# Kernel tuning notes

Hardware: AMD Instinct MI355X
Metric: run time of the kernel (lower is better)

The kernel has to match this reference:

```python
import jax, jax.numpy as jnp
import numpy as np

N_NODES = 100000
N_EDGES = 625000
EMB_DIM = 128
ALPHA = 0.8  # alpha in original; effective scale is alpha/2 = 0.4


def setup_inputs() -> dict:
    key = jax.random.key(0)
    k1, k2, k3, k4, k5 = jax.random.split(key, 5)
    x = jax.random.normal(k1, (N_NODES, EMB_DIM), dtype=jnp.float32)
    e = jax.random.normal(k2, (N_NODES, EMB_DIM), dtype=jnp.float32)
    hg_vals = jax.random.uniform(k3, (N_EDGES,), dtype=jnp.float32)
    hg_rows = jax.random.randint(k4, (N_EDGES,), 0, N_NODES, dtype=jnp.int32)
    hg_cols = jax.random.randint(k5, (N_EDGES,), 0, N_NODES, dtype=jnp.int32)
    t = jnp.zeros((), dtype=jnp.float32)
    return {"t": t, "x": x, "e": e, "hg_vals": hg_vals,
            "hg_rows": hg_rows, "hg_cols": hg_cols}


def reference(t, x, e, hg_vals, hg_rows, hg_cols):
    # f = spmm((alpha/2) * HG, x) - x + e, with alpha = 0.8 (constant per entry)
    n = x.shape[0]
    scale = ALPHA / 2.0
    # gather source node features per nonzero, scale by edge value
    msgs = (scale * hg_vals)[:, None] * x[hg_cols]          # [nnz, d]
    prop = jax.ops.segment_sum(msgs, hg_rows, num_segments=n)  # [N, d]
    return prop - x + e
```

## Files before the change

### kernel.cpp

```cpp
#include <hip/hip_runtime.h>
#include <hip/hip_fp16.h>


#define EMB_DIM 128
#define Q_SLOTS 32
#define CAP 16
#define OVF_MAX 8192
#define EPT 8

struct __align__(8) half4_t { __half2 a, b; };
typedef float f32x4 __attribute__((ext_vector_type(4)));
typedef unsigned long long u64;

__global__ void prep_kernel(const int* __restrict__ rows,
                            const int* __restrict__ cols,
                            const float* __restrict__ vals,
                            int* __restrict__ counts,
                            u64* __restrict__ slots,
                            int* __restrict__ ovf_cursor,
                            int4* __restrict__ ovf, int n_edges,
                            const f32x4* __restrict__ x4,
                            half4_t* __restrict__ xh4, int n_x4,
                            int bin_blocks)
{
    if ((int)blockIdx.x < bin_blocks) {
        const int T = bin_blocks * 256;
        const int t = blockIdx.x * 256 + threadIdx.x;
        for (int i0 = t; i0 < n_edges; i0 += T * EPT) {
            int   r[EPT], c[EPT];
            float v[EPT];
            bool  ok[EPT];
#pragma unroll
            for (int k = 0; k < EPT; ++k) {
                int i = i0 + k * T;
                ok[k] = (i < n_edges);
                if (ok[k]) { r[k] = rows[i]; c[k] = cols[i]; v[k] = vals[i]; }
            }
            int pos[EPT];
#pragma unroll
            for (int k = 0; k < EPT; ++k)
                if (ok[k]) pos[k] = atomicAdd(&counts[r[k]], 1);
#pragma unroll
            for (int k = 0; k < EPT; ++k) {
                if (!ok[k]) continue;
                u64 pv = (u64)(unsigned)c[k] |
                         ((u64)(unsigned)__float_as_int(0.4f * v[k]) << 32);
                if (pos[k] < CAP) {
                    slots[(size_t)r[k] * CAP + pos[k]] = pv;
                } else {
                    int o = atomicAdd(ovf_cursor, 1);
                    if (o < OVF_MAX)
                        ovf[o] = make_int4(r[k], c[k],
                                           __float_as_int(0.4f * v[k]), 0);
                }
            }
        }
    } else {
        long long j = ((long long)(blockIdx.x - bin_blocks) * 256 +
                       threadIdx.x) * 2;
        if (j < n_x4) {
            f32x4 f0 = x4[j];
            half4_t h0;
            h0.a = __floats2half2_rn(f0.x, f0.y);
            h0.b = __floats2half2_rn(f0.z, f0.w);
            xh4[j] = h0;
            if (j + 1 < n_x4) {
                f32x4 f1 = x4[j + 1];
                half4_t h1;
                h1.a = __floats2half2_rn(f1.x, f1.y);
                h1.b = __floats2half2_rn(f1.z, f1.w);
                xh4[j + 1] = h1;
            }
        }
    }
}

__global__ void gather_kernel(const half4_t* __restrict__ xh4,
                              const f32x4* __restrict__ e4,
                              const int* __restrict__ counts,
                              const u64* __restrict__ slots,
                              const int* __restrict__ ovf_cursor,
                              const int4* __restrict__ ovf,
                              f32x4* __restrict__ out4, int n_nodes)
{
    int tid = blockIdx.x * blockDim.x + threadIdx.x;
    int row = tid >> 5;
    int q   = tid & 31;
    if (row >= n_nodes) return;

    int cfull = counts[row];
    int n = (cfull < CAP) ? cfull : CAP;
    const u64* b = slots + (size_t)row * CAP;

    u64 pp = 0;
    if (q < n) pp = __builtin_nontemporal_load(b + q);
    int myc = (int)(pp & 0xffffffffULL);
    int myv = (int)(pp >> 32);

    float4 acc = make_float4(0.f, 0.f, 0.f, 0.f);
    int nm1 = n - 1;

    for (int base = 0; base < n; base += 8) {
        int   col[8];
        float v[8];
#pragma unroll
        for (int k = 0; k < 8; ++k) {
            int j  = base + k;
            int jc = (j < n) ? j : nm1;
            col[k] = __shfl(myc, jc, 32);
            int vi = __shfl(myv, jc, 32);
            v[k]   = (j < n) ? __int_as_float(vi) : 0.f;
        }
        half4_t hv[8];
#pragma unroll
        for (int k = 0; k < 8; ++k) {
            hv[k] = xh4[col[k] * Q_SLOTS + q];
        }
#pragma unroll
        for (int k = 0; k < 8; ++k) {
            float2 f0 = __half22float2(hv[k].a);
            float2 f1 = __half22float2(hv[k].b);
            acc.x = fmaf(v[k], f0.x, acc.x);
            acc.y = fmaf(v[k], f0.y, acc.y);
            acc.z = fmaf(v[k], f1.x, acc.z);
            acc.w = fmaf(v[k], f1.y, acc.w);
        }
    }

    if (cfull > CAP) {
        int cnt = *ovf_cursor;
        cnt = (cnt < OVF_MAX) ? cnt : OVF_MAX;
        for (int k = 0; k < cnt; ++k) {
            int4 en = ovf[k];
            if (en.x == row) {
                float vv = __int_as_float(en.z);
                half4_t hv = xh4[en.y * Q_SLOTS + q];
                float2 f0 = __half22float2(hv.a);
                float2 f1 = __half22float2(hv.b);
                acc.x = fmaf(vv, f0.x, acc.x);
                acc.y = fmaf(vv, f0.y, acc.y);
                acc.z = fmaf(vv, f1.x, acc.z);
                acc.w = fmaf(vv, f1.y, acc.w);
            }
        }
    }

    int idx = row * Q_SLOTS + q;
    half4_t hx = xh4[idx];
    float2 x0 = __half22float2(hx.a);
    float2 x1 = __half22float2(hx.b);
    f32x4 er = __builtin_nontemporal_load(e4 + idx);
    f32x4 o;
    o.x = acc.x + er.x - x0.x;
    o.y = acc.y + er.y - x0.y;
    o.z = acc.z + er.z - x1.x;
    o.w = acc.w + er.w - x1.y;
    __builtin_nontemporal_store(o, out4 + idx);
}

__global__ void build_chain_kernel(const int* __restrict__ rows,
                                   const int* __restrict__ cols,
                                   const float* __restrict__ vals,
                                   int* __restrict__ head,
                                   int4* __restrict__ nodes, int n_edges) {
    int i = blockIdx.x * blockDim.x + threadIdx.x;
    if (i >= n_edges) return;
    int r = rows[i];
    int prev = atomicExch(&head[r], i);
    nodes[i] = make_int4(cols[i], __float_as_int(0.4f * vals[i]), prev, 0);
}
__global__ void gather_chain_kernel(const float2* __restrict__ x2,
                                    const float2* __restrict__ e2,
                                    const int* __restrict__ head,
                                    const int4* __restrict__ nodes,
                                    float2* __restrict__ out2, int n_nodes) {
    int tid = blockIdx.x * blockDim.x + threadIdx.x;
    int row = tid >> 6, q = tid & 63;
    if (row >= n_nodes) return;
    float2 acc = make_float2(0.f, 0.f);
    int j = head[row];
    if (j >= 0) {
        int4 nd = nodes[j];
        for (;;) {
            int4 nd2;
            bool more = (nd.z >= 0);
            if (more) nd2 = nodes[nd.z];
            float v = __int_as_float(nd.y);
            float2 xv = x2[nd.x * 64 + q];
            acc.x = fmaf(v, xv.x, acc.x);
            acc.y = fmaf(v, xv.y, acc.y);
            if (!more) break;
            nd = nd2;
        }
    }
    int idx = row * 64 + q;
    float2 xr = x2[idx], er = e2[idx];
    out2[idx] = make_float2(acc.x + er.x - xr.x, acc.y + er.y - xr.y);
}

extern "C" void kernel_launch(void* const* d_in, const int* in_sizes, int n_in,
                              void* d_out, int out_size, void* d_ws, size_t ws_size,
                              hipStream_t stream) {
    const float* x    = (const float*)d_in[1];
    const float* e    = (const float*)d_in[2];
    const float* vals = (const float*)d_in[3];
    const int*   rows = (const int*)d_in[4];
    const int*   cols = (const int*)d_in[5];
    float* out = (float*)d_out;

    const int n_edges = in_sizes[3];
    const int n_nodes = in_sizes[1] / EMB_DIM;
    const int n_x4    = n_nodes * Q_SLOTS;

    size_t need_a = (size_t)OVF_MAX * sizeof(int4) +
                    (size_t)n_x4 * sizeof(half4_t) +
                    (size_t)n_nodes * CAP * sizeof(u64) +
                    (size_t)(n_nodes + 1) * sizeof(int);

    if (ws_size >= need_a) {
        int4*    ovf        = (int4*)d_ws;
        half4_t* xh4        = (half4_t*)(ovf + OVF_MAX);
        u64*     slots      = (u64*)(xh4 + (size_t)n_x4);
        int*     counts     = (int*)(slots + (size_t)n_nodes * CAP);
        int*     ovf_cursor = counts + n_nodes;

        hipMemsetAsync(counts, 0, (size_t)(n_nodes + 1) * sizeof(int), stream);

        int bin_blocks = (n_edges + 256 * EPT - 1) / (256 * EPT);
        int cvt_items  = (n_x4 + 1) / 2;
        int cvt_blocks = (cvt_items + 255) / 256;
        prep_kernel<<<bin_blocks + cvt_blocks, 256, 0, stream>>>(
            rows, cols, vals, counts, slots, ovf_cursor, ovf, n_edges,
            (const f32x4*)x, xh4, n_x4, bin_blocks);

        long long gt = (long long)n_nodes * 32;
        int gb = (int)((gt + 255) / 256);
        gather_kernel<<<gb, 256, 0, stream>>>(xh4, (const f32x4*)e,
                                              counts, slots,
                                              ovf_cursor, ovf,
                                              (f32x4*)out, n_nodes);
    } else {
        int4* nodes = (int4*)d_ws;
        int*  head  = (int*)(nodes + n_edges);
        hipMemsetAsync(head, 0xFF, (size_t)n_nodes * sizeof(int), stream);
        int eb = (n_edges + 255) / 256;
        build_chain_kernel<<<eb, 256, 0, stream>>>(rows, cols, vals, head,
                                                   nodes, n_edges);
        long long gt = (long long)n_nodes * 64;
        int gb = (int)((gt + 255) / 256);
        gather_chain_kernel<<<gb, 256, 0, stream>>>((const float2*)x,
                                                    (const float2*)e,
                                                    head, nodes,
                                                    (float2*)out, n_nodes);
    }
}
```

Baseline: 215.4 us.

## Simplify prep kernel to one edge and one x4 per thread, drop nontemporal loads

Replaces the batched 8-edges-per-thread binning loop and the separate conversion blocks with a single flat grid in which each thread converts one x4 element and bins at most one edge. It also switches the slot and e loads in the gather kernel from nontemporal to ordinary loads. The aim is simpler code and more threads in flight for the atomics. The cost is less memory-level parallelism per thread for the atomic batching and possibly worse cache behaviour for streamed data.

```diff
diff --git a/kernel.cpp b/kernel.cpp
--- a/kernel.cpp
+++ b/kernel.cpp
@@ -6,7 +6,6 @@
 #define Q_SLOTS 32
 #define CAP 16
 #define OVF_MAX 8192
-#define EPT 8
 
 struct __align__(8) half4_t { __half2 a, b; };
 typedef float f32x4 __attribute__((ext_vector_type(4)));
@@ -20,57 +19,29 @@
                             int* __restrict__ ovf_cursor,
                             int4* __restrict__ ovf, int n_edges,
                             const f32x4* __restrict__ x4,
-                            half4_t* __restrict__ xh4, int n_x4,
-                            int bin_blocks)
+                            half4_t* __restrict__ xh4, int n_x4)
 {
-    if ((int)blockIdx.x < bin_blocks) {
-        const int T = bin_blocks * 256;
-        const int t = blockIdx.x * 256 + threadIdx.x;
-        for (int i0 = t; i0 < n_edges; i0 += T * EPT) {
-            int   r[EPT], c[EPT];
-            float v[EPT];
-            bool  ok[EPT];
-#pragma unroll
-            for (int k = 0; k < EPT; ++k) {
-                int i = i0 + k * T;
-                ok[k] = (i < n_edges);
-                if (ok[k]) { r[k] = rows[i]; c[k] = cols[i]; v[k] = vals[i]; }
-            }
-            int pos[EPT];
-#pragma unroll
-            for (int k = 0; k < EPT; ++k)
-                if (ok[k]) pos[k] = atomicAdd(&counts[r[k]], 1);
-#pragma unroll
-            for (int k = 0; k < EPT; ++k) {
-                if (!ok[k]) continue;
-                u64 pv = (u64)(unsigned)c[k] |
-                         ((u64)(unsigned)__float_as_int(0.4f * v[k]) << 32);
-                if (pos[k] < CAP) {
-                    slots[(size_t)r[k] * CAP + pos[k]] = pv;
-                } else {
-                    int o = atomicAdd(ovf_cursor, 1);
-                    if (o < OVF_MAX)
-                        ovf[o] = make_int4(r[k], c[k],
-                                           __float_as_int(0.4f * v[k]), 0);
-                }
-            }
-        }
-    } else {
-        long long j = ((long long)(blockIdx.x - bin_blocks) * 256 +
-                       threadIdx.x) * 2;
-        if (j < n_x4) {
-            f32x4 f0 = x4[j];
-            half4_t h0;
-            h0.a = __floats2half2_rn(f0.x, f0.y);
-            h0.b = __floats2half2_rn(f0.z, f0.w);
-            xh4[j] = h0;
-            if (j + 1 < n_x4) {
-                f32x4 f1 = x4[j + 1];
-                half4_t h1;
-                h1.a = __floats2half2_rn(f1.x, f1.y);
-                h1.b = __floats2half2_rn(f1.z, f1.w);
-                xh4[j + 1] = h1;
-            }
+    int i = blockIdx.x * blockDim.x + threadIdx.x;
+    if (i < n_x4) {
+        f32x4 f = x4[i];
+        half4_t h;
+        h.a = __floats2half2_rn(f.x, f.y);
+        h.b = __floats2half2_rn(f.z, f.w);
+        xh4[i] = h;
+    }
+    if (i < n_edges) {
+        int   r  = rows[i];
+        int   c  = cols[i];
+        float vv = vals[i];
+        u64 pv = (u64)(unsigned)c |
+                 ((u64)(unsigned)__float_as_int(0.4f * vv) << 32);
+        int pos = atomicAdd(&counts[r], 1);
+        if (pos < CAP) {
+            slots[(size_t)r * CAP + pos] = pv;
+        } else {
+            int o = atomicAdd(ovf_cursor, 1);
+            if (o < OVF_MAX)
+                ovf[o] = make_int4(r, c, __float_as_int(0.4f * vv), 0);
         }
     }
 }
@@ -93,7 +64,7 @@
     const u64* b = slots + (size_t)row * CAP;
 
     u64 pp = 0;
-    if (q < n) pp = __builtin_nontemporal_load(b + q);
+    if (q < n) pp = b[q];
     int myc = (int)(pp & 0xffffffffULL);
     int myv = (int)(pp >> 32);
 
@@ -149,7 +120,7 @@
     half4_t hx = xh4[idx];
     float2 x0 = __half22float2(hx.a);
     float2 x1 = __half22float2(hx.b);
-    f32x4 er = __builtin_nontemporal_load(e4 + idx);
+    f32x4 er = e4[idx];
     f32x4 o;
     o.x = acc.x + er.x - x0.x;
     o.y = acc.y + er.y - x0.y;
@@ -226,12 +197,11 @@
 
         hipMemsetAsync(counts, 0, (size_t)(n_nodes + 1) * sizeof(int), stream);
 
-        int bin_blocks = (n_edges + 256 * EPT - 1) / (256 * EPT);
-        int cvt_items  = (n_x4 + 1) / 2;
-        int cvt_blocks = (cvt_items + 255) / 256;
-        prep_kernel<<<bin_blocks + cvt_blocks, 256, 0, stream>>>(
-            rows, cols, vals, counts, slots, ovf_cursor, ovf, n_edges,
-            (const f32x4*)x, xh4, n_x4, bin_blocks);
+        int pt = (n_x4 > n_edges) ? n_x4 : n_edges;
+        int pb = (pt + 255) / 256;
+        prep_kernel<<<pb, 256, 0, stream>>>(rows, cols, vals, counts, slots,
+                                            ovf_cursor, ovf, n_edges,
+                                            (const f32x4*)x, xh4, n_x4);
 
         long long gt = (long long)n_nodes * 32;
         int gb = (int)((gt + 255) / 256);
```

After: 216.9 us. About the same (+0.7%).
